# Kernel optimization log

Measured on AMD Instinct MI355X. Metric: run time of the kernel, lower is better.

## Reference

```python
import jax, jax.numpy as jnp
import numpy as np

D_MODEL = 1024
HEADS = 16
HEAD_DIM = D_MODEL // HEADS


def setup_inputs() -> dict:
    key = jax.random.key(0)
    ks = jax.random.split(key, 9)
    s = 1.0 / np.sqrt(D_MODEL)
    inp = {
        "inputs": jax.random.normal(ks[0], (4, 2048, D_MODEL), dtype=jnp.float32),
        "Wq": jax.random.normal(ks[1], (D_MODEL, D_MODEL), dtype=jnp.float32) * s,
        "bq": jnp.zeros((D_MODEL,), dtype=jnp.float32),
        "Wk": jax.random.normal(ks[2], (D_MODEL, D_MODEL), dtype=jnp.float32) * s,
        "bk": jnp.zeros((D_MODEL,), dtype=jnp.float32),
        "Wv": jax.random.normal(ks[3], (D_MODEL, D_MODEL), dtype=jnp.float32) * s,
        "bv": jnp.zeros((D_MODEL,), dtype=jnp.float32),
        "Wo": jax.random.normal(ks[4], (D_MODEL, D_MODEL), dtype=jnp.float32) * s,
        "bo": jnp.zeros((D_MODEL,), dtype=jnp.float32),
    }
    return inp


def reference(inputs, Wq, bq, Wk, bk, Wv, bv, Wo, bo):
    bs, seq, _ = inputs.shape
    # projections -> [b, h, s, d]
    def split_heads(x):
        return x.reshape(bs, seq, HEADS, HEAD_DIM).transpose(0, 2, 1, 3)
    q = split_heads(inputs @ Wq + bq)
    k = split_heads(inputs @ Wk + bk)
    v = split_heads(inputs @ Wv + bv)
    # NOTE: original code divides by (head_dim ** 1 / 2) == head_dim/2, not sqrt(head_dim)
    scale = HEAD_DIM / 2.0
    scores = jnp.einsum("bhqd,bhkd->bhqk", q, k) / scale
    attn = jax.nn.softmax(scores, axis=-1)
    out = jnp.einsum("bhqk,bhkd->bhqd", attn, v)
    out = out.transpose(0, 2, 1, 3).reshape(bs, seq, HEADS * HEAD_DIM)
    return out @ Wo + bo
```

## Files before the change

kernel.cpp:

```cpp
#include <hip/hip_runtime.h>
#include <stdint.h>

typedef __attribute__((ext_vector_type(8))) short bf16x8;
typedef __attribute__((ext_vector_type(4))) float f32x4;
typedef __attribute__((address_space(1))) void as1_void;
typedef __attribute__((address_space(3))) void as3_void;

#define D_MODEL 1024
#define SEQ     2048
#define BATCH   4
#define HEADS   16
#define HDIM    64

#define QSCALE 0.045084220029218407f

__device__ __forceinline__ ushort f2bf(float f) {
  union { float f; unsigned u; } v; v.f = f;
  unsigned u = v.u + 0x7fffu + ((v.u >> 16) & 1u);
  return (ushort)(u >> 16);
}

__device__ __forceinline__ void gload_lds16(const void* g, void* l) {
  __builtin_amdgcn_global_load_lds((as1_void*)(uintptr_t)g, (as3_void*)l, 16, 0, 0);
}

__device__ __forceinline__ bf16x8 pack8(float a0, float a1, float a2, float a3,
                                        float a4, float a5, float a6, float a7) {
  union { uint u[4]; bf16x8 v; } x;
  x.u[0] = __builtin_amdgcn_perm(__float_as_uint(a1), __float_as_uint(a0), 0x07060302);
  x.u[1] = __builtin_amdgcn_perm(__float_as_uint(a3), __float_as_uint(a2), 0x07060302);
  x.u[2] = __builtin_amdgcn_perm(__float_as_uint(a5), __float_as_uint(a4), 0x07060302);
  x.u[3] = __builtin_amdgcn_perm(__float_as_uint(a7), __float_as_uint(a6), 0x07060302);
  return x.v;
}

__global__ void prep_kernel(const float* __restrict__ X,
                            const float* w0, const float* w1, const float* w2, const float* w3,
                            const float* __restrict__ bq, const float* __restrict__ bk,
                            const float* __restrict__ bv,
                            ushort* __restrict__ Xb, ushort* __restrict__ WT,
                            float* __restrict__ bcat) {
  __shared__ float tile[32][33];
  const int bx = blockIdx.x, t = threadIdx.x;
  if (bx < 8192) {
    int i = bx * 256 + t;
    float4 f = reinterpret_cast<const float4*>(X)[i];
    ushort4 o;
    o.x = f2bf(f.x); o.y = f2bf(f.y); o.z = f2bf(f.z); o.w = f2bf(f.w);
    reinterpret_cast<ushort4*>(Xb)[i] = o;
  } else if (bx < 12288) {
    int tz = bx - 8192;
    int z = tz >> 10;
    int xy = tz & 1023;
    int bxt = xy & 31, byt = xy >> 5;
    const float* w = (z == 0) ? w0 : (z == 1) ? w1 : (z == 2) ? w2 : w3;
    const float sc = (z == 0) ? QSCALE : 1.0f;
    ushort* o = WT + (size_t)z * D_MODEL * D_MODEL;
    int tx = t & 31, ty = t >> 5;
    int x = bxt * 32 + tx;
    int y0 = byt * 32;
    #pragma unroll
    for (int i = ty; i < 32; i += 8)
      tile[i][tx] = w[(size_t)(y0 + i) * D_MODEL + x];
    __syncthreads();
    #pragma unroll
    for (int i = ty; i < 32; i += 8)
      o[(size_t)(bxt * 32 + i) * D_MODEL + y0 + tx] = f2bf(tile[tx][i] * sc);
  } else {
    int i = (bx - 12288) * 256 + t;
    bcat[i] = (i < 1024) ? bq[i] * QSCALE : (i < 2048) ? bk[i - 1024] : bv[i - 2048];
  }
}

#define MFMA16(a, b, c) __builtin_amdgcn_mfma_f32_16x16x32_bf16(a, b, c, 0, 0, 0)

template <int BN, bool F32OUT>
__global__ __launch_bounds__(512, 2) void gemm8p(const ushort* __restrict__ A,
                                                 const ushort* __restrict__ BT,
                                                 const float* __restrict__ bias,
                                                 ushort* __restrict__ QK,
                                                 ushort* __restrict__ Vt,
                                                 float* __restrict__ Cf) {
  constexpr int NI = BN / 64;
  constexpr int BB = BN * 128;
  constexpr int WCOL = BN / 4;
  __shared__ __align__(16) char smem[65536 + 2 * BB];
  const int tid  = threadIdx.x;
  const int w    = tid >> 6;
  const int lane = tid & 63;
  const int lo   = lane & 15, quad = lane >> 4;
  const int wr   = w >> 2, wc = w & 3;

  const int nx   = gridDim.x;
  const int nwg  = nx * gridDim.y;
  const int orig = blockIdx.y * nx + blockIdx.x;
  const int wg   = (orig & 7) * (nwg >> 3) + (orig >> 3);
  const int m0   = (wg / nx) * 256;
  const int n0   = (wg % nx) * BN;

  const int tl = tid ^ ((tid >> 3) & 7);
  const ushort* sA = A  + (size_t)(m0 + (tl >> 3)) * 1024 + (tl & 7) * 8;
  const ushort* sB = BT + (size_t)(n0 + (tl >> 3)) * 1024 + (tl & 7) * 8;
  char* lwA = smem + w * 1024;
  char* lwB = smem + 65536 + w * 1024;

  const int o0 = (quad * 16) ^ ((lo & 7) << 4);
  const int o1 = o0 ^ 64;
  const int rdA = wr * 16384 + lo * 128;
  const int rdB = 65536 + (wc * WCOL + lo) * 128;

  f32x4 acc[8][NI];
  #pragma unroll
  for (int i = 0; i < 8; ++i)
    #pragma unroll
    for (int j = 0; j < NI; ++j) acc[i][j] = {0.f, 0.f, 0.f, 0.f};

  gload_lds16(sB,               lwB);
  gload_lds16(sB +  64 * 1024,  lwB +  8192);
  if constexpr (NI == 3) gload_lds16(sB + 128 * 1024, lwB + 16384);
  gload_lds16(sA,               lwA);
  gload_lds16(sA + 128 * 1024,  lwA + 16384);
  gload_lds16(sA +  64 * 1024,  lwA +  8192);
  gload_lds16(sA + 192 * 1024,  lwA + 24576);
  asm volatile("s_waitcnt vmcnt(2)" ::: "memory");
  __builtin_amdgcn_s_barrier();
  asm volatile("" ::: "memory");

  const char* L = smem;
  #pragma unroll 2
  for (int kt = 0; kt < 16; ++kt) {
    const int b32A = (kt & 1) << 15;
    const int b32B = (kt & 1) * BB;
    const int nbA  = b32A ^ 32768;
    const int nbB  = b32B ^ BB;
    const int kc   = (kt + 1) * 64;
    const bool pf  = kt < 15;
    bf16x8 bfr[NI][2], af0[2], af1[2];

    #pragma unroll
    for (int ni = 0; ni < NI; ++ni) {
      bfr[ni][0] = *(const bf16x8*)(L + b32B + rdB + ni * 2048 + o0);
      bfr[ni][1] = *(const bf16x8*)(L + b32B + rdB + ni * 2048 + o1);
    }
    af0[0] = *(const bf16x8*)(L + b32A + rdA + o0);
    af0[1] = *(const bf16x8*)(L + b32A + rdA + o1);
    af1[0] = *(const bf16x8*)(L + b32A + rdA + 2048 + o0);
    af1[1] = *(const bf16x8*)(L + b32A + rdA + 2048 + o1);
    if (pf) {
      gload_lds16(sB + kc,             lwB + nbB);
      gload_lds16(sB + 64 * 1024 + kc, lwB + nbB + 8192);
    }
    asm volatile("s_waitcnt lgkmcnt(8)" ::: "memory");
    __builtin_amdgcn_s_barrier();
    asm volatile("s_waitcnt lgkmcnt(0)" ::: "memory");
    __builtin_amdgcn_sched_barrier(0);
    __builtin_amdgcn_s_setprio(1);
    #pragma unroll
    for (int ks = 0; ks < 2; ++ks)
      #pragma unroll
      for (int ni = 0; ni < NI; ++ni) {
        acc[0][ni] = MFMA16(af0[ks], bfr[ni][ks], acc[0][ni]);
        acc[1][ni] = MFMA16(af1[ks], bfr[ni][ks], acc[1][ni]);
      }
    __builtin_amdgcn_s_setprio(0);
    __builtin_amdgcn_s_barrier();
    asm volatile("" ::: "memory");

    af0[0] = *(const bf16x8*)(L + b32A + rdA + 2 * 2048 + o0);
    af0[1] = *(const bf16x8*)(L + b32A + rdA + 2 * 2048 + o1);
    af1[0] = *(const bf16x8*)(L + b32A + rdA + 3 * 2048 + o0);
    af1[1] = *(const bf16x8*)(L + b32A + rdA + 3 * 2048 + o1);
    if (pf) {
      if constexpr (NI == 3) {
        gload_lds16(sB + 128 * 1024 + kc, lwB + nbB + 16384);
        gload_lds16(sA + kc,              lwA + nbA);
      } else {
        gload_lds16(sA + kc,              lwA + nbA);
        gload_lds16(sA + 128 * 1024 + kc, lwA + nbA + 16384);
      }
    }
    __builtin_amdgcn_s_barrier();
    asm volatile("s_waitcnt lgkmcnt(0)" ::: "memory");
    __builtin_amdgcn_sched_barrier(0);
    __builtin_amdgcn_s_setprio(1);
    #pragma unroll
    for (int ks = 0; ks < 2; ++ks)
      #pragma unroll
      for (int ni = 0; ni < NI; ++ni) {
        acc[2][ni] = MFMA16(af0[ks], bfr[ni][ks], acc[2][ni]);
        acc[3][ni] = MFMA16(af1[ks], bfr[ni][ks], acc[3][ni]);
      }
    __builtin_amdgcn_s_setprio(0);
    if (pf) asm volatile("s_waitcnt vmcnt(4)" ::: "memory");
    else    asm volatile("s_waitcnt vmcnt(0)" ::: "memory");
    __builtin_amdgcn_s_barrier();
    asm volatile("" ::: "memory");

    af0[0] = *(const bf16x8*)(L + b32A + rdA + 4 * 2048 + o0);
    af0[1] = *(const bf16x8*)(L + b32A + rdA + 4 * 2048 + o1);
    af1[0] = *(const bf16x8*)(L + b32A + rdA + 5 * 2048 + o0);
    af1[1] = *(const bf16x8*)(L + b32A + rdA + 5 * 2048 + o1);
    if (pf) {
      if constexpr (NI == 3)
        gload_lds16(sA + 128 * 1024 + kc, lwA + nbA + 16384);
      else
        gload_lds16(sA + 64 * 1024 + kc,  lwA + nbA + 8192);
    }
    __builtin_amdgcn_s_barrier();
    asm volatile("s_waitcnt lgkmcnt(0)" ::: "memory");
    __builtin_amdgcn_sched_barrier(0);
    __builtin_amdgcn_s_setprio(1);
    #pragma unroll
    for (int ks = 0; ks < 2; ++ks)
      #pragma unroll
      for (int ni = 0; ni < NI; ++ni) {
        acc[4][ni] = MFMA16(af0[ks], bfr[ni][ks], acc[4][ni]);
        acc[5][ni] = MFMA16(af1[ks], bfr[ni][ks], acc[5][ni]);
      }
    __builtin_amdgcn_s_setprio(0);
    __builtin_amdgcn_s_barrier();
    asm volatile("" ::: "memory");

    af0[0] = *(const bf16x8*)(L + b32A + rdA + 6 * 2048 + o0);
    af0[1] = *(const bf16x8*)(L + b32A + rdA + 6 * 2048 + o1);
    af1[0] = *(const bf16x8*)(L + b32A + rdA + 7 * 2048 + o0);
    af1[1] = *(const bf16x8*)(L + b32A + rdA + 7 * 2048 + o1);
    if (pf) {
      if constexpr (NI == 3) {
        gload_lds16(sA + 64 * 1024 + kc,  lwA + nbA + 8192);
        gload_lds16(sA + 192 * 1024 + kc, lwA + nbA + 24576);
      } else {
        gload_lds16(sA + 192 * 1024 + kc, lwA + nbA + 24576);
      }
    }
    __builtin_amdgcn_s_barrier();
    asm volatile("s_waitcnt lgkmcnt(0)" ::: "memory");
    __builtin_amdgcn_sched_barrier(0);
    __builtin_amdgcn_s_setprio(1);
    #pragma unroll
    for (int ks = 0; ks < 2; ++ks)
      #pragma unroll
      for (int ni = 0; ni < NI; ++ni) {
        acc[6][ni] = MFMA16(af0[ks], bfr[ni][ks], acc[6][ni]);
        acc[7][ni] = MFMA16(af1[ks], bfr[ni][ks], acc[7][ni]);
      }
    __builtin_amdgcn_s_setprio(0);
    if (pf) asm volatile("s_waitcnt vmcnt(2)" ::: "memory");
    __builtin_amdgcn_s_barrier();
    asm volatile("" ::: "memory");
  }

  if constexpr (F32OUT) {
    #pragma unroll
    for (int ni = 0; ni < NI; ++ni) {
      const int col = n0 + wc * WCOL + ni * 16 + lo;
      const float bv = bias[col];
      #pragma unroll
      for (int mi = 0; mi < 8; ++mi) {
        const int row = m0 + wr * 128 + mi * 16 + quad * 4;
        #pragma unroll
        for (int r = 0; r < 4; ++r)
          Cf[(size_t)(row + r) * 1024 + col] = acc[mi][ni][r] + bv;
      }
    }
  } else {
    #pragma unroll
    for (int ni = 0; ni < NI; ++ni) {
      const int colb = n0 + wc * WCOL + ni * 16;
      const float bv = bias[colb + lo];
      if (colb < 2048) {
        const int col = colb + lo;
        #pragma unroll
        for (int mi = 0; mi < 8; ++mi) {
          const int row = m0 + wr * 128 + mi * 16 + quad * 4;
          #pragma unroll
          for (int r = 0; r < 4; ++r)
            QK[(size_t)(row + r) * 2048 + col] = f2bf(acc[mi][ni][r] + bv);
        }
      } else {
        const int vcol = colb + lo - 2048;
        const int hh = vcol >> 6, d = vcol & 63;
        #pragma unroll
        for (int mi = 0; mi < 8; ++mi) {
          const int base = m0 + wr * 128 + mi * 16;
          const int brow = base + quad * 4;
          const int bidx = brow >> 11;
          const int srow = brow & 2047;
          const int ck   = srow >> 6;
          const int c0   = (base & 32) + (quad << 3) + ((base >> 2) & 4);
          ushort e0 = f2bf(acc[mi][ni][0] + bv);
          ushort e1 = f2bf(acc[mi][ni][1] + bv);
          ushort e2 = f2bf(acc[mi][ni][2] + bv);
          ushort e3 = f2bf(acc[mi][ni][3] + bv);
          uint2 pk;
          pk.x = (uint)e0 | ((uint)e1 << 16);
          pk.y = (uint)e2 | ((uint)e3 << 16);
          *(uint2*)&Vt[(size_t)((bidx * HEADS + hh) * HDIM + d) * SEQ + ck * 64 + c0] = pk;
        }
      }
    }
  }
}

__global__ __launch_bounds__(256, 2) void attn_kernel(const ushort* __restrict__ QK,
                                                      const ushort* __restrict__ Vt,
                                                      ushort* __restrict__ Og) {
  __shared__ __align__(16) ushort Ks[2][64 * 64];
  __shared__ __align__(16) ushort Vs[2][64 * 64];

  const int tid  = threadIdx.x;
  const int w    = tid >> 6, lane = tid & 63;
  const int lo   = lane & 15, quad = lane >> 4;

  const int p  = blockIdx.x + (blockIdx.y << 3) + (blockIdx.z << 7);
  const int G  = ((p >> 6) << 3) | (p & 7);
  const int h  = G & 15, b = G >> 4;
  const int qbase = ((p >> 3) & 7) * 256 + w * 64;
  const int swz = lo & 7;

  auto STAGE = [&](int buf, int ck) {
    #pragma unroll
    for (int i = 0; i < 2; ++i) {
      const int c16 = (w * 2 + i) * 64 + lane;
      const int r = c16 >> 3, ps = c16 & 7;
      const int gs = ps ^ (r & 7);
      gload_lds16(QK + (size_t)(b * SEQ + ck * 64 + r) * 2048 + 1024 + h * HDIM + gs * 8,
                  &Ks[buf][(w * 2 + i) * 512]);
      gload_lds16(Vt + (size_t)((b * HEADS + h) * HDIM + r) * SEQ + ck * 64 + gs * 8,
                  &Vs[buf][(w * 2 + i) * 512]);
    }
  };

  bf16x8 qf[4][2];
  #pragma unroll
  for (int qg = 0; qg < 4; ++qg) {
    const ushort* qp = QK + (size_t)(b * SEQ + qbase + qg * 16 + lo) * 2048 + h * HDIM;
    qf[qg][0] = *(const bf16x8*)(qp + quad * 8);
    qf[qg][1] = *(const bf16x8*)(qp + 32 + quad * 8);
  }

  f32x4 acc[4][4];
  #pragma unroll
  for (int qg = 0; qg < 4; ++qg)
    #pragma unroll
    for (int t = 0; t < 4; ++t) acc[qg][t] = {0.f, 0.f, 0.f, 0.f};
  float lsum[4] = {0.f, 0.f, 0.f, 0.f};

  STAGE(0, 0);
  __syncthreads();

  #pragma unroll 2
  for (int ck = 0; ck < SEQ / 64; ++ck) {
    const int cur = ck & 1;
    if (ck < SEQ / 64 - 1) {
      STAGE(cur ^ 1, ck + 1);
      asm volatile("s_waitcnt vmcnt(4)" ::: "memory");
    } else {
      asm volatile("s_waitcnt vmcnt(0)" ::: "memory");
    }
    __builtin_amdgcn_s_barrier();
    asm volatile("" ::: "memory");

    bf16x8 kf[4][2];
    #pragma unroll
    for (int sub = 0; sub < 4; ++sub) {
      const ushort* kr = &Ks[cur][(sub * 16 + lo) * 64];
      kf[sub][0] = *(const bf16x8*)(kr + ((quad ^ swz) * 8));
      kf[sub][1] = *(const bf16x8*)(kr + (((4 + quad) ^ swz) * 8));
    }

    bf16x8 af[4][2];
    #pragma unroll
    for (int qg = 0; qg < 4; ++qg) {
      f32x4 s[4];
      #pragma unroll
      for (int sub = 0; sub < 4; ++sub) s[sub] = {0.f, 0.f, 0.f, 0.f};
      #pragma unroll
      for (int sub = 0; sub < 4; ++sub) {
        s[sub] = __builtin_amdgcn_mfma_f32_16x16x32_bf16(kf[sub][0], qf[qg][0], s[sub], 0, 0, 0);
        s[sub] = __builtin_amdgcn_mfma_f32_16x16x32_bf16(kf[sub][1], qf[qg][1], s[sub], 0, 0, 0);
      }
      float p2[4][4];
      #pragma unroll
      for (int sub = 0; sub < 4; ++sub)
        #pragma unroll
        for (int r = 0; r < 4; ++r) p2[sub][r] = __builtin_amdgcn_exp2f(s[sub][r]);
      float t0 = 0.f;
      #pragma unroll
      for (int sub = 0; sub < 4; ++sub)
        t0 += (p2[sub][0] + p2[sub][1]) + (p2[sub][2] + p2[sub][3]);
      lsum[qg] += t0;
      af[qg][0] = pack8(p2[0][0], p2[0][1], p2[0][2], p2[0][3], p2[1][0], p2[1][1], p2[1][2], p2[1][3]);
      af[qg][1] = pack8(p2[2][0], p2[2][1], p2[2][2], p2[2][3], p2[3][0], p2[3][1], p2[3][2], p2[3][3]);
    }

    __builtin_amdgcn_s_setprio(1);
    #pragma unroll
    for (int t = 0; t < 4; ++t) {
      const ushort* vr = &Vs[cur][(t * 16 + lo) * 64];
      #pragma unroll
      for (int hh = 0; hh < 2; ++hh) {
        bf16x8 vf = *(const bf16x8*)(vr + (((hh * 4 + quad) ^ swz) * 8));
        #pragma unroll
        for (int qg = 0; qg < 4; ++qg)
          acc[qg][t] = __builtin_amdgcn_mfma_f32_16x16x32_bf16(af[qg][hh], vf, acc[qg][t], 0, 0, 0);
      }
    }
    __builtin_amdgcn_s_setprio(0);

    asm volatile("" ::: "memory");
    __builtin_amdgcn_s_barrier();
    asm volatile("" ::: "memory");
  }

  #pragma unroll
  for (int qg = 0; qg < 4; ++qg) {
    float v = lsum[qg];
    v += __shfl_xor(v, 16);
    v += __shfl_xor(v, 32);
    float linv[4];
    #pragma unroll
    for (int r = 0; r < 4; ++r) linv[r] = 1.0f / __shfl(v, quad * 4 + r);
    #pragma unroll
    for (int t = 0; t < 4; ++t)
      #pragma unroll
      for (int r = 0; r < 4; ++r)
        Og[(size_t)(b * SEQ + qbase + qg * 16 + quad * 4 + r) * D_MODEL + h * HDIM + t * 16 + lo] =
            f2bf(acc[qg][t][r] * linv[r]);
  }
}

extern "C" void kernel_launch(void* const* d_in, const int* in_sizes, int n_in,
                              void* d_out, int out_size, void* d_ws, size_t ws_size,
                              hipStream_t stream) {
  const float* X  = (const float*)d_in[0];
  const float* Wq = (const float*)d_in[1];
  const float* bq = (const float*)d_in[2];
  const float* Wk = (const float*)d_in[3];
  const float* bk = (const float*)d_in[4];
  const float* Wv = (const float*)d_in[5];
  const float* bv = (const float*)d_in[6];
  const float* Wo = (const float*)d_in[7];
  const float* bo = (const float*)d_in[8];
  float* out = (float*)d_out;
  char* ws = (char*)d_ws;

  ushort* Xb  = (ushort*)(ws);
  ushort* WT  = (ushort*)(ws + 16777216);
  ushort* QKb = (ushort*)(ws + 25165824);
  ushort* Vtb = (ushort*)(ws + 58720256);
  ushort* Ob  = (ushort*)(ws + 75497472);
  float*  bcat = (float*)(ws + 75497472);
  const int WSTRIDE = D_MODEL * D_MODEL;

  prep_kernel<<<12300, 256, 0, stream>>>(X, Wq, Wk, Wv, Wo, bq, bk, bv, Xb, WT, bcat);

  gemm8p<192, false><<<dim3(16, 32), 512, 0, stream>>>(Xb, WT, bcat, QKb, Vtb, nullptr);

  attn_kernel<<<dim3(SEQ / 256, HEADS, BATCH), 256, 0, stream>>>(QKb, Vtb, Ob);

  gemm8p<128, true><<<dim3(8, 32), 512, 0, stream>>>(Ob, WT + 3 * WSTRIDE, bo, nullptr, nullptr, out);
}
```

Baseline: 249.9 us.

## Software-pipeline attention loop so PV MFMAs overlap next chunk's QK and exp

Restructures the attention inner loop into a two-stage software pipeline. Each iteration computes QK scores and exp for the current KV chunk, then runs the PV MFMAs for the previous chunk using probabilities and V fragments held in registers. This lets the matrix unit and the transcendental/VALU work of independent chunks interleave, hiding the dependency from exp to PV. The cost is more live registers (an extra af/vf set), a prologue and an epilogue, and possible occupancy loss or spills.

```diff
diff --git a/kernel.cpp b/kernel.cpp
--- a/kernel.cpp
+++ b/kernel.cpp
@@ -347,10 +347,59 @@
   float lsum[4] = {0.f, 0.f, 0.f, 0.f};
 
   STAGE(0, 0);
-  __syncthreads();
+  STAGE(1, 1);
+  asm volatile("s_waitcnt vmcnt(4)" ::: "memory");
+  __builtin_amdgcn_s_barrier();
+  asm volatile("" ::: "memory");
+
+  bf16x8 afP[4][2];
+  bf16x8 vfP[4][2];
+
+  {
+    bf16x8 kf[4][2];
+    #pragma unroll
+    for (int sub = 0; sub < 4; ++sub) {
+      const ushort* kr = &Ks[0][(sub * 16 + lo) * 64];
+      kf[sub][0] = *(const bf16x8*)(kr + ((quad ^ swz) * 8));
+      kf[sub][1] = *(const bf16x8*)(kr + (((4 + quad) ^ swz) * 8));
+    }
+    #pragma unroll
+    for (int qg = 0; qg < 4; ++qg) {
+      f32x4 s[4];
+      #pragma unroll
+      for (int sub = 0; sub < 4; ++sub) s[sub] = {0.f, 0.f, 0.f, 0.f};
+      #pragma unroll
+      for (int sub = 0; sub < 4; ++sub) {
+        s[sub] = MFMA16(kf[sub][0], qf[qg][0], s[sub]);
+        s[sub] = MFMA16(kf[sub][1], qf[qg][1], s[sub]);
+      }
+      float p2[4][4];
+      #pragma unroll
+      for (int sub = 0; sub < 4; ++sub)
+        #pragma unroll
+        for (int r = 0; r < 4; ++r) p2[sub][r] = __builtin_amdgcn_exp2f(s[sub][r]);
+      float t0 = 0.f;
+      #pragma unroll
+      for (int sub = 0; sub < 4; ++sub)
+        t0 += (p2[sub][0] + p2[sub][1]) + (p2[sub][2] + p2[sub][3]);
+      lsum[qg] += t0;
+      afP[qg][0] = pack8(p2[0][0], p2[0][1], p2[0][2], p2[0][3], p2[1][0], p2[1][1], p2[1][2], p2[1][3]);
+      afP[qg][1] = pack8(p2[2][0], p2[2][1], p2[2][2], p2[2][3], p2[3][0], p2[3][1], p2[3][2], p2[3][3]);
+    }
+    #pragma unroll
+    for (int t = 0; t < 4; ++t) {
+      const ushort* vr = &Vs[0][(t * 16 + lo) * 64];
+      #pragma unroll
+      for (int hh = 0; hh < 2; ++hh)
+        vfP[t][hh] = *(const bf16x8*)(vr + (((hh * 4 + quad) ^ swz) * 8));
+    }
+  }
+  asm volatile("" ::: "memory");
+  __builtin_amdgcn_s_barrier();
+  asm volatile("" ::: "memory");
 
   #pragma unroll 2
-  for (int ck = 0; ck < SEQ / 64; ++ck) {
+  for (int ck = 1; ck < SEQ / 64; ++ck) {
     const int cur = ck & 1;
     if (ck < SEQ / 64 - 1) {
       STAGE(cur ^ 1, ck + 1);
@@ -369,7 +418,8 @@
       kf[sub][1] = *(const bf16x8*)(kr + (((4 + quad) ^ swz) * 8));
     }
 
-    bf16x8 af[4][2];
+    bf16x8 afC[4][2], vfC[4][2];
+    __builtin_amdgcn_s_setprio(1);
     #pragma unroll
     for (int qg = 0; qg < 4; ++qg) {
       f32x4 s[4];
@@ -377,8 +427,8 @@
       for (int sub = 0; sub < 4; ++sub) s[sub] = {0.f, 0.f, 0.f, 0.f};
       #pragma unroll
       for (int sub = 0; sub < 4; ++sub) {
-        s[sub] = __builtin_amdgcn_mfma_f32_16x16x32_bf16(kf[sub][0], qf[qg][0], s[sub], 0, 0, 0);
-        s[sub] = __builtin_amdgcn_mfma_f32_16x16x32_bf16(kf[sub][1], qf[qg][1], s[sub], 0, 0, 0);
+        s[sub] = MFMA16(kf[sub][0], qf[qg][0], s[sub]);
+        s[sub] = MFMA16(kf[sub][1], qf[qg][1], s[sub]);
       }
       float p2[4][4];
       #pragma unroll
@@ -390,28 +440,44 @@
       for (int sub = 0; sub < 4; ++sub)
         t0 += (p2[sub][0] + p2[sub][1]) + (p2[sub][2] + p2[sub][3]);
       lsum[qg] += t0;
-      af[qg][0] = pack8(p2[0][0], p2[0][1], p2[0][2], p2[0][3], p2[1][0], p2[1][1], p2[1][2], p2[1][3]);
-      af[qg][1] = pack8(p2[2][0], p2[2][1], p2[2][2], p2[2][3], p2[3][0], p2[3][1], p2[3][2], p2[3][3]);
-    }
-
-    __builtin_amdgcn_s_setprio(1);
+      afC[qg][0] = pack8(p2[0][0], p2[0][1], p2[0][2], p2[0][3], p2[1][0], p2[1][1], p2[1][2], p2[1][3]);
+      afC[qg][1] = pack8(p2[2][0], p2[2][1], p2[2][2], p2[2][3], p2[3][0], p2[3][1], p2[3][2], p2[3][3]);
+    }
+
     #pragma unroll
     for (int t = 0; t < 4; ++t) {
       const ushort* vr = &Vs[cur][(t * 16 + lo) * 64];
       #pragma unroll
-      for (int hh = 0; hh < 2; ++hh) {
-        bf16x8 vf = *(const bf16x8*)(vr + (((hh * 4 + quad) ^ swz) * 8));
+      for (int hh = 0; hh < 2; ++hh)
+        vfC[t][hh] = *(const bf16x8*)(vr + (((hh * 4 + quad) ^ swz) * 8));
+    }
+
+    #pragma unroll
+    for (int t = 0; t < 4; ++t)
+      #pragma unroll
+      for (int hh = 0; hh < 2; ++hh)
         #pragma unroll
         for (int qg = 0; qg < 4; ++qg)
-          acc[qg][t] = __builtin_amdgcn_mfma_f32_16x16x32_bf16(af[qg][hh], vf, acc[qg][t], 0, 0, 0);
-      }
-    }
+          acc[qg][t] = MFMA16(afP[qg][hh], vfP[t][hh], acc[qg][t]);
     __builtin_amdgcn_s_setprio(0);
 
-    asm volatile("" ::: "memory");
-    __builtin_amdgcn_s_barrier();
-    asm volatile("" ::: "memory");
-  }
+    #pragma unroll
+    for (int qg = 0; qg < 4; ++qg) { afP[qg][0] = afC[qg][0]; afP[qg][1] = afC[qg][1]; }
+    #pragma unroll
+    for (int t = 0; t < 4; ++t) { vfP[t][0] = vfC[t][0]; vfP[t][1] = vfC[t][1]; }
+
+    asm volatile("" ::: "memory");
+    __builtin_amdgcn_s_barrier();
+    asm volatile("" ::: "memory");
+  }
+
+  #pragma unroll
+  for (int t = 0; t < 4; ++t)
+    #pragma unroll
+    for (int hh = 0; hh < 2; ++hh)
+      #pragma unroll
+      for (int qg = 0; qg < 4; ++qg)
+        acc[qg][t] = MFMA16(afP[qg][hh], vfP[t][hh], acc[qg][t]);
 
   #pragma unroll
   for (int qg = 0; qg < 4; ++qg) {
```

New measurement: 268.5 us. +7.4%, slower.

## Replace 8-wave 256-row GEMM with 4-wave 128x128 tile two-phase pipeline

Applied to the files above, without the earlier changes.

Both projection GEMMs now use a 256-thread, 4-wave kernel with 128x128 output tiles and a 2x2 wave layout, each wave computing 64x64, instead of 512-thread blocks with 256-row tiles. The main loop drops from four barrier-separated phases to two, with fewer barriers per k-step, and the grids grow to 24x64 and 8x64 blocks. The intent is to raise the block count and occupancy and cut synchronisation overhead. The cost is more global/L2 traffic per output element, since the smaller tiles get less operand reuse.

```diff
diff --git a/kernel.cpp b/kernel.cpp
--- a/kernel.cpp
+++ b/kernel.cpp
@@ -75,53 +75,52 @@
 #define MFMA16(a, b, c) __builtin_amdgcn_mfma_f32_16x16x32_bf16(a, b, c, 0, 0, 0)
 
 template <int BN, bool F32OUT>
-__global__ __launch_bounds__(512, 2) void gemm8p(const ushort* __restrict__ A,
+__global__ __launch_bounds__(256, 2) void gemm2p(const ushort* __restrict__ A,
                                                  const ushort* __restrict__ BT,
                                                  const float* __restrict__ bias,
                                                  ushort* __restrict__ QK,
                                                  ushort* __restrict__ Vt,
                                                  float* __restrict__ Cf) {
-  constexpr int NI = BN / 64;
+  static_assert(BN == 128, "gemm2p tuned for BN=128");
   constexpr int BB = BN * 128;
-  constexpr int WCOL = BN / 4;
-  __shared__ __align__(16) char smem[65536 + 2 * BB];
+  __shared__ __align__(16) char smem[32768 + 2 * BB];
   const int tid  = threadIdx.x;
-  const int w    = tid >> 6;
-  const int lane = tid & 63;
+  const int w    = tid >> 6, lane = tid & 63;
   const int lo   = lane & 15, quad = lane >> 4;
-  const int wr   = w >> 2, wc = w & 3;
+  const int wr   = w >> 1, wc = w & 1;
 
   const int nx   = gridDim.x;
   const int nwg  = nx * gridDim.y;
   const int orig = blockIdx.y * nx + blockIdx.x;
   const int wg   = (orig & 7) * (nwg >> 3) + (orig >> 3);
-  const int m0   = (wg / nx) * 256;
+  const int m0   = (wg / nx) * 128;
   const int n0   = (wg % nx) * BN;
 
   const int tl = tid ^ ((tid >> 3) & 7);
   const ushort* sA = A  + (size_t)(m0 + (tl >> 3)) * 1024 + (tl & 7) * 8;
   const ushort* sB = BT + (size_t)(n0 + (tl >> 3)) * 1024 + (tl & 7) * 8;
   char* lwA = smem + w * 1024;
-  char* lwB = smem + 65536 + w * 1024;
+  char* lwB = smem + 32768 + w * 1024;
 
   const int o0 = (quad * 16) ^ ((lo & 7) << 4);
   const int o1 = o0 ^ 64;
-  const int rdA = wr * 16384 + lo * 128;
-  const int rdB = 65536 + (wc * WCOL + lo) * 128;
-
-  f32x4 acc[8][NI];
+  const int rdA = (wr * 64 + lo) * 128;
+  const int rdB = 32768 + (wc * 64 + lo) * 128;
+
+  f32x4 acc[4][4];
   #pragma unroll
-  for (int i = 0; i < 8; ++i)
-    #pragma unroll
-    for (int j = 0; j < NI; ++j) acc[i][j] = {0.f, 0.f, 0.f, 0.f};
-
-  gload_lds16(sB,               lwB);
-  gload_lds16(sB +  64 * 1024,  lwB +  8192);
-  if constexpr (NI == 3) gload_lds16(sB + 128 * 1024, lwB + 16384);
-  gload_lds16(sA,               lwA);
-  gload_lds16(sA + 128 * 1024,  lwA + 16384);
-  gload_lds16(sA +  64 * 1024,  lwA +  8192);
-  gload_lds16(sA + 192 * 1024,  lwA + 24576);
+  for (int i = 0; i < 4; ++i)
+    #pragma unroll
+    for (int j = 0; j < 4; ++j) acc[i][j] = {0.f, 0.f, 0.f, 0.f};
+
+  gload_lds16(sA,             lwA);
+  gload_lds16(sA + 32 * 1024, lwA + 4096);
+  gload_lds16(sA + 64 * 1024, lwA + 8192);
+  gload_lds16(sA + 96 * 1024, lwA + 12288);
+  gload_lds16(sB,             lwB);
+  gload_lds16(sB + 64 * 1024, lwB + 8192);
+  gload_lds16(sB + 32 * 1024, lwB + 4096);
+  gload_lds16(sB + 96 * 1024, lwB + 12288);
   asm volatile("s_waitcnt vmcnt(2)" ::: "memory");
   __builtin_amdgcn_s_barrier();
   asm volatile("" ::: "memory");
@@ -129,174 +128,124 @@
   const char* L = smem;
   #pragma unroll 2
   for (int kt = 0; kt < 16; ++kt) {
-    const int b32A = (kt & 1) << 15;
-    const int b32B = (kt & 1) * BB;
-    const int nbA  = b32A ^ 32768;
-    const int nbB  = b32B ^ BB;
-    const int kc   = (kt + 1) * 64;
-    const bool pf  = kt < 15;
-    bf16x8 bfr[NI][2], af0[2], af1[2];
-
-    #pragma unroll
-    for (int ni = 0; ni < NI; ++ni) {
-      bfr[ni][0] = *(const bf16x8*)(L + b32B + rdB + ni * 2048 + o0);
-      bfr[ni][1] = *(const bf16x8*)(L + b32B + rdB + ni * 2048 + o1);
-    }
-    af0[0] = *(const bf16x8*)(L + b32A + rdA + o0);
-    af0[1] = *(const bf16x8*)(L + b32A + rdA + o1);
-    af1[0] = *(const bf16x8*)(L + b32A + rdA + 2048 + o0);
-    af1[1] = *(const bf16x8*)(L + b32A + rdA + 2048 + o1);
+    const int bA = (kt & 1) << 14;
+    const int bB = (kt & 1) * BB;
+    const int nA = bA ^ 16384;
+    const int nB = bB ^ BB;
+    const int kc = (kt + 1) * 64;
+    const bool pf = kt < 15;
+    bf16x8 af[4][2], bfr[2][2];
+
+    #pragma unroll
+    for (int mi = 0; mi < 4; ++mi) {
+      af[mi][0] = *(const bf16x8*)(L + bA + rdA + mi * 2048 + o0);
+      af[mi][1] = *(const bf16x8*)(L + bA + rdA + mi * 2048 + o1);
+    }
+    #pragma unroll
+    for (int j = 0; j < 2; ++j) {
+      bfr[j][0] = *(const bf16x8*)(L + bB + rdB + j * 2048 + o0);
+      bfr[j][1] = *(const bf16x8*)(L + bB + rdB + j * 2048 + o1);
+    }
     if (pf) {
-      gload_lds16(sB + kc,             lwB + nbB);
-      gload_lds16(sB + 64 * 1024 + kc, lwB + nbB + 8192);
-    }
-    asm volatile("s_waitcnt lgkmcnt(8)" ::: "memory");
-    __builtin_amdgcn_s_barrier();
+      gload_lds16(sA + kc,             lwA + nA);
+      gload_lds16(sA + 32 * 1024 + kc, lwA + nA + 4096);
+      gload_lds16(sA + 64 * 1024 + kc, lwA + nA + 8192);
+      gload_lds16(sA + 96 * 1024 + kc, lwA + nA + 12288);
+      gload_lds16(sB + kc,             lwB + nB);
+      gload_lds16(sB + 64 * 1024 + kc, lwB + nB + 8192);
+    }
     asm volatile("s_waitcnt lgkmcnt(0)" ::: "memory");
     __builtin_amdgcn_sched_barrier(0);
     __builtin_amdgcn_s_setprio(1);
     #pragma unroll
     for (int ks = 0; ks < 2; ++ks)
       #pragma unroll
-      for (int ni = 0; ni < NI; ++ni) {
-        acc[0][ni] = MFMA16(af0[ks], bfr[ni][ks], acc[0][ni]);
-        acc[1][ni] = MFMA16(af1[ks], bfr[ni][ks], acc[1][ni]);
+      for (int mi = 0; mi < 4; ++mi) {
+        acc[mi][0] = MFMA16(af[mi][ks], bfr[0][ks], acc[mi][0]);
+        acc[mi][1] = MFMA16(af[mi][ks], bfr[1][ks], acc[mi][1]);
       }
     __builtin_amdgcn_s_setprio(0);
+    if (pf) asm volatile("s_waitcnt vmcnt(6)" ::: "memory");
+    else    asm volatile("s_waitcnt vmcnt(0)" ::: "memory");
     __builtin_amdgcn_s_barrier();
     asm volatile("" ::: "memory");
 
-    af0[0] = *(const bf16x8*)(L + b32A + rdA + 2 * 2048 + o0);
-    af0[1] = *(const bf16x8*)(L + b32A + rdA + 2 * 2048 + o1);
-    af1[0] = *(const bf16x8*)(L + b32A + rdA + 3 * 2048 + o0);
-    af1[1] = *(const bf16x8*)(L + b32A + rdA + 3 * 2048 + o1);
+    #pragma unroll
+    for (int j = 0; j < 2; ++j) {
+      bfr[j][0] = *(const bf16x8*)(L + bB + rdB + (2 + j) * 2048 + o0);
+      bfr[j][1] = *(const bf16x8*)(L + bB + rdB + (2 + j) * 2048 + o1);
+    }
     if (pf) {
-      if constexpr (NI == 3) {
-        gload_lds16(sB + 128 * 1024 + kc, lwB + nbB + 16384);
-        gload_lds16(sA + kc,              lwA + nbA);
-      } else {
-        gload_lds16(sA + kc,              lwA + nbA);
-        gload_lds16(sA + 128 * 1024 + kc, lwA + nbA + 16384);
-      }
-    }
-    __builtin_amdgcn_s_barrier();
+      gload_lds16(sB + 32 * 1024 + kc, lwB + nB + 4096);
+      gload_lds16(sB + 96 * 1024 + kc, lwB + nB + 12288);
+    }
     asm volatile("s_waitcnt lgkmcnt(0)" ::: "memory");
     __builtin_amdgcn_sched_barrier(0);
     __builtin_amdgcn_s_setprio(1);
     #pragma unroll
     for (int ks = 0; ks < 2; ++ks)
       #pragma unroll
-      for (int ni = 0; ni < NI; ++ni) {
-        acc[2][ni] = MFMA16(af0[ks], bfr[ni][ks], acc[2][ni]);
-        acc[3][ni] = MFMA16(af1[ks], bfr[ni][ks], acc[3][ni]);
+      for (int mi = 0; mi < 4; ++mi) {
+        acc[mi][2] = MFMA16(af[mi][ks], bfr[0][ks], acc[mi][2]);
+        acc[mi][3] = MFMA16(af[mi][ks], bfr[1][ks], acc[mi][3]);
       }
     __builtin_amdgcn_s_setprio(0);
-    if (pf) asm volatile("s_waitcnt vmcnt(4)" ::: "memory");
-    else    asm volatile("s_waitcnt vmcnt(0)" ::: "memory");
-    __builtin_amdgcn_s_barrier();
-    asm volatile("" ::: "memory");
-
-    af0[0] = *(const bf16x8*)(L + b32A + rdA + 4 * 2048 + o0);
-    af0[1] = *(const bf16x8*)(L + b32A + rdA + 4 * 2048 + o1);
-    af1[0] = *(const bf16x8*)(L + b32A + rdA + 5 * 2048 + o0);
-    af1[1] = *(const bf16x8*)(L + b32A + rdA + 5 * 2048 + o1);
     if (pf) {
-      if constexpr (NI == 3)
-        gload_lds16(sA + 128 * 1024 + kc, lwA + nbA + 16384);
-      else
-        gload_lds16(sA + 64 * 1024 + kc,  lwA + nbA + 8192);
-    }
-    __builtin_amdgcn_s_barrier();
-    asm volatile("s_waitcnt lgkmcnt(0)" ::: "memory");
-    __builtin_amdgcn_sched_barrier(0);
-    __builtin_amdgcn_s_setprio(1);
-    #pragma unroll
-    for (int ks = 0; ks < 2; ++ks)
-      #pragma unroll
-      for (int ni = 0; ni < NI; ++ni) {
-        acc[4][ni] = MFMA16(af0[ks], bfr[ni][ks], acc[4][ni]);
-        acc[5][ni] = MFMA16(af1[ks], bfr[ni][ks], acc[5][ni]);
-      }
-    __builtin_amdgcn_s_setprio(0);
-    __builtin_amdgcn_s_barrier();
-    asm volatile("" ::: "memory");
-
-    af0[0] = *(const bf16x8*)(L + b32A + rdA + 6 * 2048 + o0);
-    af0[1] = *(const bf16x8*)(L + b32A + rdA + 6 * 2048 + o1);
-    af1[0] = *(const bf16x8*)(L + b32A + rdA + 7 * 2048 + o0);
-    af1[1] = *(const bf16x8*)(L + b32A + rdA + 7 * 2048 + o1);
-    if (pf) {
-      if constexpr (NI == 3) {
-        gload_lds16(sA + 64 * 1024 + kc,  lwA + nbA + 8192);
-        gload_lds16(sA + 192 * 1024 + kc, lwA + nbA + 24576);
-      } else {
-        gload_lds16(sA + 192 * 1024 + kc, lwA + nbA + 24576);
-      }
-    }
-    __builtin_amdgcn_s_barrier();
-    asm volatile("s_waitcnt lgkmcnt(0)" ::: "memory");
-    __builtin_amdgcn_sched_barrier(0);
-    __builtin_amdgcn_s_setprio(1);
-    #pragma unroll
-    for (int ks = 0; ks < 2; ++ks)
-      #pragma unroll
-      for (int ni = 0; ni < NI; ++ni) {
-        acc[6][ni] = MFMA16(af0[ks], bfr[ni][ks], acc[6][ni]);
-        acc[7][ni] = MFMA16(af1[ks], bfr[ni][ks], acc[7][ni]);
-      }
-    __builtin_amdgcn_s_setprio(0);
-    if (pf) asm volatile("s_waitcnt vmcnt(2)" ::: "memory");
-    __builtin_amdgcn_s_barrier();
-    asm volatile("" ::: "memory");
+      asm volatile("s_waitcnt vmcnt(2)" ::: "memory");
+      __builtin_amdgcn_s_barrier();
+      asm volatile("" ::: "memory");
+    }
   }
 
   if constexpr (F32OUT) {
     #pragma unroll
-    for (int ni = 0; ni < NI; ++ni) {
-      const int col = n0 + wc * WCOL + ni * 16 + lo;
+    for (int ni = 0; ni < 4; ++ni) {
+      const int col = n0 + wc * 64 + ni * 16 + lo;
       const float bv = bias[col];
       #pragma unroll
-      for (int mi = 0; mi < 8; ++mi) {
-        const int row = m0 + wr * 128 + mi * 16 + quad * 4;
+      for (int mi = 0; mi < 4; ++mi) {
+        const int row = m0 + wr * 64 + mi * 16 + quad * 4;
         #pragma unroll
         for (int r = 0; r < 4; ++r)
           Cf[(size_t)(row + r) * 1024 + col] = acc[mi][ni][r] + bv;
       }
     }
+  } else if (n0 < 2048) {
+    #pragma unroll
+    for (int ni = 0; ni < 4; ++ni) {
+      const int col = n0 + wc * 64 + ni * 16 + lo;
+      const float bv = bias[col];
+      #pragma unroll
+      for (int mi = 0; mi < 4; ++mi) {
+        const int row = m0 + wr * 64 + mi * 16 + quad * 4;
+        #pragma unroll
+        for (int r = 0; r < 4; ++r)
+          QK[(size_t)(row + r) * 2048 + col] = f2bf(acc[mi][ni][r] + bv);
+      }
+    }
   } else {
     #pragma unroll
-    for (int ni = 0; ni < NI; ++ni) {
-      const int colb = n0 + wc * WCOL + ni * 16;
-      const float bv = bias[colb + lo];
-      if (colb < 2048) {
-        const int col = colb + lo;
-        #pragma unroll
-        for (int mi = 0; mi < 8; ++mi) {
-          const int row = m0 + wr * 128 + mi * 16 + quad * 4;
-          #pragma unroll
-          for (int r = 0; r < 4; ++r)
-            QK[(size_t)(row + r) * 2048 + col] = f2bf(acc[mi][ni][r] + bv);
-        }
-      } else {
-        const int vcol = colb + lo - 2048;
-        const int hh = vcol >> 6, d = vcol & 63;
-        #pragma unroll
-        for (int mi = 0; mi < 8; ++mi) {
-          const int base = m0 + wr * 128 + mi * 16;
-          const int brow = base + quad * 4;
-          const int bidx = brow >> 11;
-          const int srow = brow & 2047;
-          const int ck   = srow >> 6;
-          const int c0   = (base & 32) + (quad << 3) + ((base >> 2) & 4);
-          ushort e0 = f2bf(acc[mi][ni][0] + bv);
-          ushort e1 = f2bf(acc[mi][ni][1] + bv);
-          ushort e2 = f2bf(acc[mi][ni][2] + bv);
-          ushort e3 = f2bf(acc[mi][ni][3] + bv);
-          uint2 pk;
-          pk.x = (uint)e0 | ((uint)e1 << 16);
-          pk.y = (uint)e2 | ((uint)e3 << 16);
-          *(uint2*)&Vt[(size_t)((bidx * HEADS + hh) * HDIM + d) * SEQ + ck * 64 + c0] = pk;
-        }
+    for (int ni = 0; ni < 4; ++ni) {
+      const int col  = n0 + wc * 64 + ni * 16 + lo;
+      const int vcol = col - 2048;
+      const int hh = vcol >> 6, d = vcol & 63;
+      const float bv = bias[col];
+      #pragma unroll
+      for (int mi = 0; mi < 4; ++mi) {
+        const int base = m0 + wr * 64 + mi * 16;
+        const int brow = base + quad * 4;
+        const int bidx = brow >> 11;
+        const int srow = brow & 2047;
+        const int ck   = srow >> 6;
+        const int c0   = (base & 32) + (quad << 3) + ((base >> 2) & 4);
+        ushort e0 = f2bf(acc[mi][ni][0] + bv);
+        ushort e1 = f2bf(acc[mi][ni][1] + bv);
+        ushort e2 = f2bf(acc[mi][ni][2] + bv);
+        ushort e3 = f2bf(acc[mi][ni][3] + bv);
+        uint2 pk;
+        pk.x = (uint)e0 | ((uint)e1 << 16);
+        pk.y = (uint)e2 | ((uint)e3 << 16);
+        *(uint2*)&Vt[(size_t)((bidx * HEADS + hh) * HDIM + d) * SEQ + ck * 64 + c0] = pk;
       }
     }
   }
@@ -455,9 +404,9 @@
 
   prep_kernel<<<12300, 256, 0, stream>>>(X, Wq, Wk, Wv, Wo, bq, bk, bv, Xb, WT, bcat);
 
-  gemm8p<192, false><<<dim3(16, 32), 512, 0, stream>>>(Xb, WT, bcat, QKb, Vtb, nullptr);
+  gemm2p<128, false><<<dim3(24, 64), 256, 0, stream>>>(Xb, WT, bcat, QKb, Vtb, nullptr);
 
   attn_kernel<<<dim3(SEQ / 256, HEADS, BATCH), 256, 0, stream>>>(QKb, Vtb, Ob);
 
-  gemm8p<128, true><<<dim3(8, 32), 512, 0, stream>>>(Ob, WT + 3 * WSTRIDE, bo, nullptr, nullptr, out);
-}
+  gemm2p<128, true><<<dim3(8, 64), 256, 0, stream>>>(Ob, WT + 3 * WSTRIDE, bo, nullptr, nullptr, out);
+}
```

New measurement: 239.7 us. -4.1%, faster.
